# Optimization experiments

Hardware: AMD Instinct MI355X
Metric: run time of the kernel (lower is better)

The kernel has to match this reference:

```python
import jax, jax.numpy as jnp
import numpy as np

N_NODES = 50000
N_EDGES = 400000
IN_DIM = 256
HID = 64
N_CLASSES = 121


def setup_inputs() -> dict:
    key = jax.random.key(0)
    ks = jax.random.split(key, 16)
    inp = {
        "features": jax.random.normal(ks[0], (N_NODES, IN_DIM), jnp.float32),
        "src": jax.random.randint(ks[1], (N_EDGES,), 0, N_NODES, jnp.int32),
        "dst": jax.random.randint(ks[2], (N_EDGES,), 0, N_NODES, jnp.int32),
        # layer 0: 4 heads, in_dim -> hid, no residual
        "W0": jax.random.normal(ks[3], (4, HID, IN_DIM), jnp.float32) * 0.05,
        "al0": jax.random.normal(ks[4], (4, HID), jnp.float32) * 0.05,
        "ar0": jax.random.normal(ks[5], (4, HID), jnp.float32) * 0.05,
        # layer 1: 4 heads, 4*hid -> hid, residual via fc
        "W1": jax.random.normal(ks[6], (4, HID, 4 * HID), jnp.float32) * 0.05,
        "al1": jax.random.normal(ks[7], (4, HID), jnp.float32) * 0.05,
        "ar1": jax.random.normal(ks[8], (4, HID), jnp.float32) * 0.05,
        "R1": jax.random.normal(ks[9], (4, HID, 4 * HID), jnp.float32) * 0.05,
        # final: 6 heads, 4*hid -> classes, residual via fc, averaged
        "Wf": jax.random.normal(ks[10], (6, N_CLASSES, 4 * HID), jnp.float32) * 0.05,
        "alf": jax.random.normal(ks[11], (6, N_CLASSES), jnp.float32) * 0.05,
        "arf": jax.random.normal(ks[12], (6, N_CLASSES), jnp.float32) * 0.05,
        "Rf": jax.random.normal(ks[13], (6, N_CLASSES, 4 * HID), jnp.float32) * 0.05,
    }
    return inp


def _gat_layer(x, src, dst, W, al, ar, R, n_nodes):
    """Multi-head GAT layer. x:[N,D], W:[H,K,D], al/ar:[H,K], R:[H,K,D] or None.
    Returns [N,H,K] = activation(residual + edge-softmax-weighted neighbor sum)."""
    ft = jnp.einsum('nd,hkd->nhk', x, W)              # [N,H,K]
    a1 = jnp.einsum('nhk,hk->nh', ft, al)             # [N,H] attn_l(ft)
    a2 = jnp.einsum('nhk,hk->nh', ft, ar)             # [N,H] attn_r(ft)
    # per-edge score: leaky_relu(a1[dst] + a2[src]) (DGL mailbox softmax over in-edges)
    s = jax.nn.leaky_relu(a1[dst] + a2[src], negative_slope=0.01)   # [E,H]
    smax = jax.ops.segment_max(s, dst, num_segments=n_nodes)        # [N,H]
    smax = jnp.where(jnp.isfinite(smax), smax, 0.0)
    ex = jnp.exp(s - smax[dst])                                     # [E,H]
    denom = jax.ops.segment_sum(ex, dst, num_segments=n_nodes)      # [N,H]
    msg = ex[:, :, None] * ft[src]                                  # [E,H,K]
    accum = jax.ops.segment_sum(msg, dst, num_segments=n_nodes)     # [N,H,K]
    accum = accum / jnp.where(denom > 0, denom, 1.0)[:, :, None]
    if R is not None:
        accum = accum + jnp.einsum('nd,hkd->nhk', x, R)
    return jax.nn.elu(accum)


def reference(features, src, dst, W0, al0, ar0, W1, al1, ar1, R1, Wf, alf, arf, Rf):
    n = features.shape[0]
    h0 = _gat_layer(features, src, dst, W0, al0, ar0, None, n)  # [N,4,64]
    h0 = h0.reshape(n, -1)                                      # concat heads -> [N,256]
    h1 = _gat_layer(h0, src, dst, W1, al1, ar1, R1, n)          # [N,4,64]
    h1 = h1.reshape(n, -1)                                      # [N,256]
    hf = _gat_layer(h1, src, dst, Wf, alf, arf, Rf, n)          # [N,6,121]
    return hf.mean(axis=1)                                      # average final heads -> [N,121]
```

## Files before the change

### kernel.cpp

```cpp
#include <hip/hip_runtime.h>
#include <math.h>

#define NN 50000
#define NE 400000
#define NB ((NN + 255) / 256)

typedef __attribute__((ext_vector_type(8))) short bf16x8;
typedef __attribute__((ext_vector_type(4))) float f32x4;
#define AS1 __attribute__((address_space(1)))
#define AS3 __attribute__((address_space(3)))

__device__ __forceinline__ float lrelu(float x){ return x > 0.0f ? x : 0.01f*x; }
__device__ __forceinline__ float eluf(float x){ return x > 0.0f ? x : __expf(x)-1.0f; }
__device__ __forceinline__ float bf2f(unsigned short u){
  union{unsigned i; float f;} v; v.i = ((unsigned)u)<<16; return v.f;
}
__device__ __forceinline__ unsigned short f2bf(float x){
  union{float f; unsigned i;} v; v.f = x;
  unsigned r = v.i + 0x7FFFu + ((v.i>>16)&1u);
  return (unsigned short)(r>>16);
}
__device__ __forceinline__ unsigned pack2(float a, float b){
  return (unsigned)f2bf(a) | ((unsigned)f2bf(b)<<16);
}
__device__ __forceinline__ float lo16(unsigned u){ return bf2f((unsigned short)(u & 0xffffu)); }
__device__ __forceinline__ float hi16(unsigned u){ return bf2f((unsigned short)(u >> 16)); }

__global__ void k_diag(float* out, float val){ out[0] = val; }

__global__ void k_cvt(const float* __restrict__ in, unsigned short* __restrict__ o, int n){
  int i = (blockIdx.x*256 + threadIdx.x)*4;
  if(i + 3 < n){
    float4 v = *(const float4*)(in + i);
    uint2 p; p.x = pack2(v.x, v.y); p.y = pack2(v.z, v.w);
    *(uint2*)(o + i) = p;
  } else {
    for(int k = i; k < n; k++) o[k] = f2bf(in[k]);
  }
}

__global__ void k_cvt3(const float* __restrict__ s0, const float* __restrict__ s1,
    const float* __restrict__ s2, unsigned short* __restrict__ d0,
    unsigned short* __restrict__ d1, unsigned short* __restrict__ d2, int n){
  const float* in = (blockIdx.y == 0) ? s0 : (blockIdx.y == 1) ? s1 : s2;
  unsigned short* o = (blockIdx.y == 0) ? d0 : (blockIdx.y == 1) ? d1 : d2;
  int i = (blockIdx.x*256 + threadIdx.x)*4;
  if(i + 3 < n){
    float4 v = *(const float4*)(in + i);
    uint2 p; p.x = pack2(v.x, v.y); p.y = pack2(v.z, v.w);
    *(uint2*)(o + i) = p;
  } else {
    for(int k = i; k < n; k++) o[k] = f2bf(in[k]);
  }
}

__global__ void k_cvt2(const float* __restrict__ s0, const float* __restrict__ s1,
    unsigned short* __restrict__ d0, unsigned short* __restrict__ d1, int n){
  const float* in = (blockIdx.y == 0) ? s0 : s1;
  unsigned short* o = (blockIdx.y == 0) ? d0 : d1;
  int i = (blockIdx.x*256 + threadIdx.x)*4;
  if(i + 3 < n){
    float4 v = *(const float4*)(in + i);
    uint2 p; p.x = pack2(v.x, v.y); p.y = pack2(v.z, v.w);
    *(uint2*)(o + i) = p;
  } else {
    for(int k = i; k < n; k++) o[k] = f2bf(in[k]);
  }
}

__global__ void k_fold(const float* __restrict__ W, const float* __restrict__ al,
    const float* __restrict__ ar, float* __restrict__ fl, float* __restrict__ fr, int K){
  int h = blockIdx.x, d = threadIdx.x;
  float sl = 0.f, sr = 0.f;
  const float* wb = W + ((size_t)h*K)*256 + d;
  for(int k = 0; k < K; k++){
    float w = wb[(size_t)k*256];
    sl += al[h*K + k]*w;
    sr += ar[h*K + k]*w;
  }
  fl[h*256 + d] = sl;
  fr[h*256 + d] = sr;
}

__global__ void k_count(const int* __restrict__ dst, int* __restrict__ cnt, int E){
  int e = blockIdx.x * 256 + threadIdx.x;
  if(e < E) atomicAdd(&cnt[dst[e]], 1);
}

__global__ void k_scanA(const int* __restrict__ cnt, int* __restrict__ row_ptr,
    int* __restrict__ bsum, int N){
  __shared__ int sh[256];
  int t = threadIdx.x;
  int i = blockIdx.x*256 + t;
  int v = (i < N) ? cnt[i] : 0;
  sh[t] = v;
  __syncthreads();
  for(int off = 1; off < 256; off <<= 1){
    int u = (t >= off) ? sh[t - off] : 0;
    __syncthreads();
    sh[t] += u;
    __syncthreads();
  }
  if(i < N) row_ptr[i] = sh[t] - v;
  if(t == 255) bsum[blockIdx.x] = sh[255];
}

__global__ void k_scanB(const int* __restrict__ bsum, int* __restrict__ boff, int nb){
  __shared__ int sh[256];
  int t = threadIdx.x;
  int v = (t < nb) ? bsum[t] : 0;
  sh[t] = v;
  __syncthreads();
  for(int off = 1; off < 256; off <<= 1){
    int u = (t >= off) ? sh[t - off] : 0;
    __syncthreads();
    sh[t] += u;
    __syncthreads();
  }
  if(t < nb) boff[t] = sh[t] - v;
  if(t == 255) boff[nb] = sh[255];
}

__global__ void k_scanC(int* __restrict__ row_ptr, const int* __restrict__ boff, int N, int nb){
  int i = blockIdx.x*256 + threadIdx.x;
  if(i < N) row_ptr[i] += boff[blockIdx.x];
  if(i == 0) row_ptr[N] = boff[nb];
}

__global__ void k_scatter(const int* __restrict__ src, const int* __restrict__ dst,
    const int* __restrict__ row_ptr, int* __restrict__ cur, int* __restrict__ col_src, int E){
  int e = blockIdx.x * 256 + threadIdx.x;
  if(e < E){
    int d = dst[e];
    int pos = row_ptr[d] + atomicAdd(&cur[d], 1);
    col_src[pos] = src[e];
  }
}

__global__ __launch_bounds__(256) void k_gemm16(const unsigned short* __restrict__ X,
    const unsigned short* __restrict__ W, unsigned short* __restrict__ out,
    int N, int Kout, int ostride){
  __shared__ unsigned short sA[4096];
  __shared__ unsigned short sB[4096];
  int tid = threadIdx.x;
  int l = tid & 63, w = tid >> 6;
  int wm = w >> 1, wn = w & 1;
  int row0 = blockIdx.x*128, col0 = blockIdx.y*128;

  f32x4 acc[4][4];
  #pragma unroll
  for(int i=0;i<4;i++)
    #pragma unroll
    for(int j=0;j<4;j++) acc[i][j] = (f32x4){0.f,0.f,0.f,0.f};

  int grA0 = row0 + l;        if(grA0 >= N) grA0 = 0;
  int grA1 = row0 + 64 + l;   if(grA1 >= N) grA1 = 0;
  int gcB0 = col0 + l;        if(gcB0 >= Kout) gcB0 = 0;
  int gcB1 = col0 + 64 + l;   if(gcB1 >= Kout) gcB1 = 0;
  const unsigned short* pa0 = X + (size_t)grA0*256 + w*8;
  const unsigned short* pa1 = X + (size_t)grA1*256 + w*8;
  const unsigned short* pb0 = W + (size_t)gcB0*256 + w*8;
  const unsigned short* pb1 = W + (size_t)gcB1*256 + w*8;

  AS3 unsigned short* a3A = (AS3 unsigned short*)sA;
  AS3 unsigned short* a3B = (AS3 unsigned short*)sB;

  for(int kt = 0; kt < 256; kt += 32){
    __builtin_amdgcn_global_load_lds((const AS1 void*)(pa0 + kt), (AS3 void*)(a3A + w*1024),       16, 0, 0);
    __builtin_amdgcn_global_load_lds((const AS1 void*)(pa1 + kt), (AS3 void*)(a3A + w*1024 + 512), 16, 0, 0);
    __builtin_amdgcn_global_load_lds((const AS1 void*)(pb0 + kt), (AS3 void*)(a3B + w*1024),       16, 0, 0);
    __builtin_amdgcn_global_load_lds((const AS1 void*)(pb1 + kt), (AS3 void*)(a3B + w*1024 + 512), 16, 0, 0);
    __syncthreads();
    bf16x8 af[4], bfr[4];
    #pragma unroll
    for(int f=0; f<4; f++){
      af[f]  = *(const bf16x8*)(sA + (l>>4)*1024 + (wm*64 + f*16 + (l&15))*8);
      bfr[f] = *(const bf16x8*)(sB + (l>>4)*1024 + (wn*64 + f*16 + (l&15))*8);
    }
    #pragma unroll
    for(int i=0;i<4;i++)
      #pragma unroll
      for(int j=0;j<4;j++)
        acc[i][j] = __builtin_amdgcn_mfma_f32_16x16x32_bf16(af[i], bfr[j], acc[i][j], 0, 0, 0);
    __syncthreads();
  }

  #pragma unroll
  for(int i=0;i<4;i++){
    int rbase = row0 + wm*64 + i*16 + (l>>4)*4;
    #pragma unroll
    for(int j=0;j<4;j++){
      int c = col0 + wn*64 + j*16 + (l&15);
      if(c < Kout){
        #pragma unroll
        for(int q=0;q<4;q++){
          int r = rbase + q;
          if(r < N) out[(size_t)r*ostride + c] = f2bf(acc[i][j][q]);
        }
      }
    }
  }
}

__global__ __launch_bounds__(256) void k_gemmFh(const unsigned short* __restrict__ aggX,
    const unsigned short* __restrict__ xin, const unsigned short* __restrict__ wf,
    const unsigned short* __restrict__ rf, float* __restrict__ partial, int M){
  __shared__ unsigned short sA[4096];
  __shared__ unsigned short sB[4096];
  int tid = threadIdx.x;
  int l = tid & 63, w = tid >> 6;
  int wm = w >> 1, wn = w & 1;
  int h = blockIdx.y;
  int row0 = blockIdx.x*128;
  int rA0 = row0 + l;      if(rA0 >= M) rA0 = 0;
  int rA1 = row0 + 64 + l; if(rA1 >= M) rA1 = 0;
  int cB1 = 64 + l; if(cB1 > 120) cB1 = 120;

  AS3 unsigned short* a3A = (AS3 unsigned short*)sA;
  AS3 unsigned short* a3B = (AS3 unsigned short*)sB;

  f32x4 acc[4][4];
  #pragma unroll
  for(int i=0;i<4;i++)
    #pragma unroll
    for(int j=0;j<4;j++) acc[i][j] = (f32x4){0.f,0.f,0.f,0.f};

  #pragma unroll 1
  for(int ph = 0; ph < 2; ph++){
    const unsigned short* pa0 = (ph ? xin + (size_t)rA0*256 : aggX + (size_t)rA0*1536 + h*256) + w*8;
    const unsigned short* pa1 = (ph ? xin + (size_t)rA1*256 : aggX + (size_t)rA1*1536 + h*256) + w*8;
    const unsigned short* pbb = (ph ? rf : wf) + (size_t)h*121*256;
    const unsigned short* pb0 = pbb + (size_t)l*256 + w*8;
    const unsigned short* pb1 = pbb + (size_t)cB1*256 + w*8;
    for(int kt = 0; kt < 256; kt += 32){
      __builtin_amdgcn_global_load_lds((const AS1 void*)(pa0 + kt), (AS3 void*)(a3A + w*1024),       16, 0, 0);
      __builtin_amdgcn_global_load_lds((const AS1 void*)(pa1 + kt), (AS3 void*)(a3A + w*1024 + 512), 16, 0, 0);
      __builtin_amdgcn_global_load_lds((const AS1 void*)(pb0 + kt), (AS3 void*)(a3B + w*1024),       16, 0, 0);
      __builtin_amdgcn_global_load_lds((const AS1 void*)(pb1 + kt), (AS3 void*)(a3B + w*1024 + 512), 16, 0, 0);
      __syncthreads();
      bf16x8 af[4], bfr[4];
      #pragma unroll
      for(int f=0; f<4; f++){
        af[f]  = *(const bf16x8*)(sA + (l>>4)*1024 + (wm*64 + f*16 + (l&15))*8);
        bfr[f] = *(const bf16x8*)(sB + (l>>4)*1024 + (wn*64 + f*16 + (l&15))*8);
      }
      #pragma unroll
      for(int i=0;i<4;i++)
        #pragma unroll
        for(int j=0;j<4;j++)
          acc[i][j] = __builtin_amdgcn_mfma_f32_16x16x32_bf16(af[i], bfr[j], acc[i][j], 0, 0, 0);
      __syncthreads();
    }
  }

  float* pb = partial + (size_t)h*M*128;
  #pragma unroll
  for(int i=0;i<4;i++){
    int rbase = row0 + wm*64 + i*16 + (l>>4)*4;
    #pragma unroll
    for(int j=0;j<4;j++){
      int c = wn*64 + j*16 + (l&15);
      #pragma unroll
      for(int q=0;q<4;q++){
        int r = rbase + q;
        if(r < M) pb[(size_t)r*128 + c] = eluf(acc[i][j][q]);
      }
    }
  }
}

__global__ __launch_bounds__(256) void k_reduce6(const float* __restrict__ partial,
    float* __restrict__ outp, int n0, int M){
  int t = blockIdx.x*256 + threadIdx.x;
  int idx = t >> 7, c = t & 127;
  if(idx >= M || c >= 121) return;
  float s = 0.f;
  #pragma unroll
  for(int h = 0; h < 6; h++) s += partial[((size_t)h*M + idx)*128 + c];
  outp[(size_t)(n0 + idx)*121 + c] = s * (1.0f/6.0f);
}

template<int H, int OS>
__global__ __launch_bounds__(256) void k_a12dot(const unsigned short* __restrict__ x,
    const float* __restrict__ fl, const float* __restrict__ fr,
    float* __restrict__ a1, float* __restrict__ a2){
  int n = blockIdx.x*4 + (threadIdx.x>>6);
  if(n >= NN) return;
  int l = threadIdx.x & 63;
  uint2 rv = *(const uint2*)(x + (size_t)n*256 + l*4);
  float c0 = lo16(rv.x), c1 = hi16(rv.x), c2 = lo16(rv.y), c3 = hi16(rv.y);
  float s1[H], s2[H];
  #pragma unroll
  for(int h = 0; h < H; h++){
    float4 vl = *(const float4*)(fl + h*256 + l*4);
    float4 vr = *(const float4*)(fr + h*256 + l*4);
    s1[h] = c0*vl.x + c1*vl.y + c2*vl.z + c3*vl.w;
    s2[h] = c0*vr.x + c1*vr.y + c2*vr.z + c3*vr.w;
  }
  #pragma unroll
  for(int off = 32; off > 0; off >>= 1){
    #pragma unroll
    for(int h = 0; h < H; h++){
      s1[h] += __shfl_xor(s1[h], off);
      s2[h] += __shfl_xor(s2[h], off);
    }
  }
  if(l == 0){
    #pragma unroll
    for(int h = 0; h < H; h++){ a1[(size_t)n*OS + h] = s1[h]; a2[(size_t)n*OS + h] = s2[h]; }
  }
}

template<bool HAS_RES>
__global__ __launch_bounds__(256) void k_agg4(const unsigned short* __restrict__ ft, int fts,
    const float* __restrict__ a1, const float* __restrict__ a2,
    const int* __restrict__ row_ptr, const int* __restrict__ col_src,
    const unsigned short* __restrict__ res, int rs, unsigned short* __restrict__ outp){
  int n = blockIdx.x*4 + (threadIdx.x>>6);
  if(n >= NN) return;
  int l = threadIdx.x & 63;
  int h = l >> 4;
  int e0 = row_ptr[n], e1 = row_ptr[n+1];
  float a1v = a1[n*4 + h];
  float acc0=0.f, acc1=0.f, acc2=0.f, acc3=0.f, d=0.f;
  int e = e0;
  for(; e + 4 <= e1; e += 4){
    int s0 = col_src[e], s1 = col_src[e+1], s2 = col_src[e+2], s3 = col_src[e+3];
    float sc0 = a2[(size_t)s0*4 + h];
    float sc1 = a2[(size_t)s1*4 + h];
    float sc2 = a2[(size_t)s2*4 + h];
    float sc3 = a2[(size_t)s3*4 + h];
    uint2 r0 = *(const uint2*)(ft + (size_t)s0*fts + l*4);
    uint2 r1 = *(const uint2*)(ft + (size_t)s1*fts + l*4);
    uint2 r2 = *(const uint2*)(ft + (size_t)s2*fts + l*4);
    uint2 r3 = *(const uint2*)(ft + (size_t)s3*fts + l*4);
    float x0 = __expf(lrelu(a1v + sc0));
    float x1 = __expf(lrelu(a1v + sc1));
    float x2 = __expf(lrelu(a1v + sc2));
    float x3 = __expf(lrelu(a1v + sc3));
    d += (x0 + x1) + (x2 + x3);
    acc0 += x0*lo16(r0.x) + x1*lo16(r1.x) + x2*lo16(r2.x) + x3*lo16(r3.x);
    acc1 += x0*hi16(r0.x) + x1*hi16(r1.x) + x2*hi16(r2.x) + x3*hi16(r3.x);
    acc2 += x0*lo16(r0.y) + x1*lo16(r1.y) + x2*lo16(r2.y) + x3*lo16(r3.y);
    acc3 += x0*hi16(r0.y) + x1*hi16(r1.y) + x2*hi16(r2.y) + x3*hi16(r3.y);
  }
  for(; e < e1; ++e){
    int s = col_src[e];
    float x = __expf(lrelu(a1v + a2[(size_t)s*4 + h]));
    d += x;
    uint2 rv = *(const uint2*)(ft + (size_t)s*fts + l*4);
    acc0 += x*lo16(rv.x); acc1 += x*hi16(rv.x);
    acc2 += x*lo16(rv.y); acc3 += x*hi16(rv.y);
  }
  float inv = (e1 > e0) ? 1.0f/d : 0.0f;
  float v0 = acc0*inv, v1 = acc1*inv, v2 = acc2*inv, v3 = acc3*inv;
  if(HAS_RES){
    uint2 rr = *(const uint2*)(res + (size_t)n*rs + l*4);
    v0 += lo16(rr.x); v1 += hi16(rr.x); v2 += lo16(rr.y); v3 += hi16(rr.y);
  }
  uint2 o;
  o.x = pack2(eluf(v0), eluf(v1));
  o.y = pack2(eluf(v2), eluf(v3));
  *(uint2*)(outp + (size_t)n*256 + l*4) = o;
}

__global__ __launch_bounds__(256) void k_aggx6(const unsigned short* __restrict__ x,
    const float* __restrict__ a1, const float* __restrict__ a2,
    const int* __restrict__ row_ptr, const int* __restrict__ col_src,
    unsigned short* __restrict__ aggX, int n0base, int M){
  int idx = blockIdx.x*4 + (threadIdx.x>>6);
  if(idx >= M) return;
  int n = n0base + idx;
  int l = threadIdx.x & 63;
  int e0 = row_ptr[n], e1 = row_ptr[n+1];
  float a1v[6];
  #pragma unroll
  for(int h=0;h<6;h++) a1v[h] = a1[(size_t)n*8 + h];
  float acc[6][4];
  float d[6];
  #pragma unroll
  for(int h=0;h<6;h++){ d[h]=0.f; acc[h][0]=0.f; acc[h][1]=0.f; acc[h][2]=0.f; acc[h][3]=0.f; }
  int e = e0;
  for(; e + 2 <= e1; e += 2){
    int s0 = col_src[e], s1 = col_src[e+1];
    float4 alo0 = *(const float4*)(a2 + (size_t)s0*8);
    float2 ahi0 = *(const float2*)(a2 + (size_t)s0*8 + 4);
    float4 alo1 = *(const float4*)(a2 + (size_t)s1*8);
    float2 ahi1 = *(const float2*)(a2 + (size_t)s1*8 + 4);
    uint2 rv0 = *(const uint2*)(x + (size_t)s0*256 + l*4);
    uint2 rv1 = *(const uint2*)(x + (size_t)s1*256 + l*4);
    float ex0[6], ex1[6];
    ex0[0] = __expf(lrelu(a1v[0] + alo0.x));
    ex0[1] = __expf(lrelu(a1v[1] + alo0.y));
    ex0[2] = __expf(lrelu(a1v[2] + alo0.z));
    ex0[3] = __expf(lrelu(a1v[3] + alo0.w));
    ex0[4] = __expf(lrelu(a1v[4] + ahi0.x));
    ex0[5] = __expf(lrelu(a1v[5] + ahi0.y));
    ex1[0] = __expf(lrelu(a1v[0] + alo1.x));
    ex1[1] = __expf(lrelu(a1v[1] + alo1.y));
    ex1[2] = __expf(lrelu(a1v[2] + alo1.z));
    ex1[3] = __expf(lrelu(a1v[3] + alo1.w));
    ex1[4] = __expf(lrelu(a1v[4] + ahi1.x));
    ex1[5] = __expf(lrelu(a1v[5] + ahi1.y));
    float c00 = lo16(rv0.x), c01 = hi16(rv0.x), c02 = lo16(rv0.y), c03 = hi16(rv0.y);
    float c10 = lo16(rv1.x), c11 = hi16(rv1.x), c12 = lo16(rv1.y), c13 = hi16(rv1.y);
    #pragma unroll
    for(int h=0;h<6;h++){
      d[h] += ex0[h] + ex1[h];
      acc[h][0] += ex0[h]*c00 + ex1[h]*c10;
      acc[h][1] += ex0[h]*c01 + ex1[h]*c11;
      acc[h][2] += ex0[h]*c02 + ex1[h]*c12;
      acc[h][3] += ex0[h]*c03 + ex1[h]*c13;
    }
  }
  for(; e < e1; ++e){
    int s = col_src[e];
    float4 alo = *(const float4*)(a2 + (size_t)s*8);
    float2 ahi = *(const float2*)(a2 + (size_t)s*8 + 4);
    uint2 rv = *(const uint2*)(x + (size_t)s*256 + l*4);
    float ex[6];
    ex[0] = __expf(lrelu(a1v[0] + alo.x));
    ex[1] = __expf(lrelu(a1v[1] + alo.y));
    ex[2] = __expf(lrelu(a1v[2] + alo.z));
    ex[3] = __expf(lrelu(a1v[3] + alo.w));
    ex[4] = __expf(lrelu(a1v[4] + ahi.x));
    ex[5] = __expf(lrelu(a1v[5] + ahi.y));
    float c0 = lo16(rv.x), c1 = hi16(rv.x), c2 = lo16(rv.y), c3 = hi16(rv.y);
    #pragma unroll
    for(int h=0;h<6;h++){
      d[h] += ex[h];
      acc[h][0] += ex[h]*c0;
      acc[h][1] += ex[h]*c1;
      acc[h][2] += ex[h]*c2;
      acc[h][3] += ex[h]*c3;
    }
  }
  bool deg = e1 > e0;
  #pragma unroll
  for(int h=0;h<6;h++){
    float inv = deg ? 1.0f/d[h] : 0.0f;
    uint2 o;
    o.x = pack2(acc[h][0]*inv, acc[h][1]*inv);
    o.y = pack2(acc[h][2]*inv, acc[h][3]*inv);
    *(uint2*)(aggX + (size_t)idx*1536 + h*256 + l*4) = o;
  }
}

extern "C" void kernel_launch(void* const* d_in, const int* in_sizes, int n_in,
                              void* d_out, int out_size, void* d_ws, size_t ws_size,
                              hipStream_t stream){
  const float* features = (const float*)d_in[0];
  const int*   src      = (const int*)d_in[1];
  const int*   dst      = (const int*)d_in[2];
  const float* W0  = (const float*)d_in[3];
  const float* al0 = (const float*)d_in[4];
  const float* ar0 = (const float*)d_in[5];
  const float* W1  = (const float*)d_in[6];
  const float* al1 = (const float*)d_in[7];
  const float* ar1 = (const float*)d_in[8];
  const float* R1  = (const float*)d_in[9];
  const float* Wf  = (const float*)d_in[10];
  const float* alf = (const float*)d_in[11];
  const float* arf = (const float*)d_in[12];
  const float* Rf  = (const float*)d_in[13];
  float* out = (float*)d_out;
  (void)in_sizes; (void)n_in; (void)out_size;

  char* ws = (char*)d_ws;
  size_t off = 0;
  auto take = [&](size_t bytes) -> void* {
    void* p = ws + off;
    off += (bytes + 255) & ~(size_t)255;
    return p;
  };
  const int CH = 25000;
  int* row_ptr = (int*)take((NN + 1) * sizeof(int));
  int* cur     = (int*)take(NN * sizeof(int));
  int* col_src = (int*)take(NE * sizeof(int));
  int* bsum    = (int*)take(256 * sizeof(int));
  int* boff    = (int*)take(257 * sizeof(int));
  float* a1 = (float*)take((size_t)NN * 8 * sizeof(float));
  float* a2 = (float*)take((size_t)NN * 8 * sizeof(float));
  unsigned short* ftres  = (unsigned short*)take((size_t)NN * 512 * 2);
  unsigned short* feat16 = (unsigned short*)take((size_t)NN * 256 * 2);
  unsigned short* hA16   = (unsigned short*)take((size_t)NN * 256 * 2);
  unsigned short* hB16   = (unsigned short*)take((size_t)NN * 256 * 2);
  unsigned short* aggX   = (unsigned short*)take((size_t)CH * 1536 * 2);
  unsigned short* w016  = (unsigned short*)take(65536 * 2);
  unsigned short* w1r1  = (unsigned short*)take(131072 * 2);
  unsigned short* wf16  = (unsigned short*)take(185856 * 2);
  unsigned short* rf16  = (unsigned short*)take(185856 * 2);
  float* fl0 = (float*)take(4*256*sizeof(float));
  float* fr0 = (float*)take(4*256*sizeof(float));
  float* fl1 = (float*)take(4*256*sizeof(float));
  float* fr1 = (float*)take(4*256*sizeof(float));
  float* flF = (float*)take(6*256*sizeof(float));
  float* frF = (float*)take(6*256*sizeof(float));
  size_t need = off;

  if(ws_size < need){
    k_diag<<<1, 1, 0, stream>>>(out, 100.0f + (float)((double)ws_size / 1073741824.0));
    return;
  }

  float* partialF = (float*)ftres;

  hipMemsetAsync(cur, 0, NN * sizeof(int), stream);
  k_count<<<(NE + 255)/256, 256, 0, stream>>>(dst, cur, NE);
  k_scanA<<<NB, 256, 0, stream>>>(cur, row_ptr, bsum, NN);
  k_scanB<<<1, 256, 0, stream>>>(bsum, boff, NB);
  k_scanC<<<NB, 256, 0, stream>>>(row_ptr, boff, NN, NB);
  hipMemsetAsync(cur, 0, NN * sizeof(int), stream);
  k_scatter<<<(NE + 255)/256, 256, 0, stream>>>(src, dst, row_ptr, cur, col_src, NE);

  k_cvt<<<(NN*256/4 + 255)/256, 256, 0, stream>>>(features, feat16, NN*256);
  k_cvt3<<<dim3(64, 3), 256, 0, stream>>>(W0, W1, R1, w016, w1r1, w1r1 + 65536, 65536);
  k_cvt2<<<dim3(182, 2), 256, 0, stream>>>(Wf, Rf, wf16, rf16, 185856);
  k_fold<<<4, 256, 0, stream>>>(W0, al0, ar0, fl0, fr0, 64);
  k_fold<<<4, 256, 0, stream>>>(W1, al1, ar1, fl1, fr1, 64);
  k_fold<<<6, 256, 0, stream>>>(Wf, alf, arf, flF, frF, 121);

  int gm = (NN + 127) / 128;
  int gagg = (NN + 3) / 4;

  k_a12dot<4,4><<<gagg, 256, 0, stream>>>(feat16, fl0, fr0, a1, a2);
  k_gemm16<<<dim3(gm, 2), 256, 0, stream>>>(feat16, w016, ftres, NN, 256, 256);
  k_agg4<false><<<gagg, 256, 0, stream>>>(ftres, 256, a1, a2, row_ptr, col_src, nullptr, 0, hA16);

  k_a12dot<4,4><<<gagg, 256, 0, stream>>>(hA16, fl1, fr1, a1, a2);
  k_gemm16<<<dim3(gm, 4), 256, 0, stream>>>(hA16, w1r1, ftres, NN, 512, 512);
  k_agg4<true><<<gagg, 256, 0, stream>>>(ftres, 512, a1, a2, row_ptr, col_src, ftres + 256, 512, hB16);

  k_a12dot<6,8><<<gagg, 256, 0, stream>>>(hB16, flF, frF, a1, a2);
  for(int c = 0; c < 2; c++){
    int n0 = c*CH;
    k_aggx6<<<(CH + 3)/4, 256, 0, stream>>>(hB16, a1, a2, row_ptr, col_src, aggX, n0, CH);
    k_gemmFh<<<dim3((CH + 127)/128, 6), 256, 0, stream>>>(aggX, hB16 + (size_t)n0*256, wf16, rf16, partialF, CH);
    k_reduce6<<<(CH*128 + 255)/256, 256, 0, stream>>>(partialF, out, n0, CH);
  }
}
```

Baseline: 605.2 us.

## Fuse next-layer attention dots into aggregation; bf16 partials; merge fold kernels

The next layer's attention logits (a1/a2) are now computed inside the aggregation kernel from the fp32 ELU outputs, removing two separate a12dot passes that re-read the 256-wide bf16 features. Double-buffered a1/a2 arrays avoid a read/write hazard between layers. The final-head partial results are stored as bf16 instead of fp32, halving that write and the reduce-kernel read at some cost in precision. The three fold launches are merged into one.

Measured after the change: 517.7 us. 1.17x faster.

```diff
diff --git a/kernel.cpp b/kernel.cpp
--- a/kernel.cpp
+++ b/kernel.cpp
@@ -68,9 +68,16 @@
   }
 }
 
-__global__ void k_fold(const float* __restrict__ W, const float* __restrict__ al,
-    const float* __restrict__ ar, float* __restrict__ fl, float* __restrict__ fr, int K){
-  int h = blockIdx.x, d = threadIdx.x;
+__global__ void k_foldAll(const float* __restrict__ W0, const float* __restrict__ al0, const float* __restrict__ ar0,
+    const float* __restrict__ W1, const float* __restrict__ al1, const float* __restrict__ ar1,
+    const float* __restrict__ Wf, const float* __restrict__ alf, const float* __restrict__ arf,
+    float* __restrict__ fl0, float* __restrict__ fr0, float* __restrict__ fl1, float* __restrict__ fr1,
+    float* __restrict__ flF, float* __restrict__ frF){
+  int b = blockIdx.x, d = threadIdx.x;
+  const float *W, *al, *ar; float *fl, *fr; int K, h;
+  if(b < 4){ W=W0; al=al0; ar=ar0; fl=fl0; fr=fr0; K=64; h=b; }
+  else if(b < 8){ W=W1; al=al1; ar=ar1; fl=fl1; fr=fr1; K=64; h=b-4; }
+  else { W=Wf; al=alf; ar=arf; fl=flF; fr=frF; K=121; h=b-8; }
   float sl = 0.f, sr = 0.f;
   const float* wb = W + ((size_t)h*K)*256 + d;
   for(int k = 0; k < K; k++){
@@ -204,7 +211,7 @@
 
 __global__ __launch_bounds__(256) void k_gemmFh(const unsigned short* __restrict__ aggX,
     const unsigned short* __restrict__ xin, const unsigned short* __restrict__ wf,
-    const unsigned short* __restrict__ rf, float* __restrict__ partial, int M){
+    const unsigned short* __restrict__ rf, unsigned short* __restrict__ partial, int M){
   __shared__ unsigned short sA[4096];
   __shared__ unsigned short sB[4096];
   int tid = threadIdx.x;
@@ -253,7 +260,7 @@
     }
   }
 
-  float* pb = partial + (size_t)h*M*128;
+  unsigned short* pb = partial + (size_t)h*M*128;
   #pragma unroll
   for(int i=0;i<4;i++){
     int rbase = row0 + wm*64 + i*16 + (l>>4)*4;
@@ -263,20 +270,20 @@
       #pragma unroll
       for(int q=0;q<4;q++){
         int r = rbase + q;
-        if(r < M) pb[(size_t)r*128 + c] = eluf(acc[i][j][q]);
+        if(r < M) pb[(size_t)r*128 + c] = f2bf(eluf(acc[i][j][q]));
       }
     }
   }
 }
 
-__global__ __launch_bounds__(256) void k_reduce6(const float* __restrict__ partial,
+__global__ __launch_bounds__(256) void k_reduce6(const unsigned short* __restrict__ partial,
     float* __restrict__ outp, int n0, int M){
   int t = blockIdx.x*256 + threadIdx.x;
   int idx = t >> 7, c = t & 127;
   if(idx >= M || c >= 121) return;
   float s = 0.f;
   #pragma unroll
-  for(int h = 0; h < 6; h++) s += partial[((size_t)h*M + idx)*128 + c];
+  for(int h = 0; h < 6; h++) s += bf2f(partial[((size_t)h*M + idx)*128 + c]);
   outp[(size_t)(n0 + idx)*121 + c] = s * (1.0f/6.0f);
 }
 
@@ -311,11 +318,13 @@
   }
 }
 
-template<bool HAS_RES>
+template<bool HAS_RES, int NH, int NOS>
 __global__ __launch_bounds__(256) void k_agg4(const unsigned short* __restrict__ ft, int fts,
     const float* __restrict__ a1, const float* __restrict__ a2,
     const int* __restrict__ row_ptr, const int* __restrict__ col_src,
-    const unsigned short* __restrict__ res, int rs, unsigned short* __restrict__ outp){
+    const unsigned short* __restrict__ res, int rs, unsigned short* __restrict__ outp,
+    const float* __restrict__ nfl, const float* __restrict__ nfr,
+    float* __restrict__ na1, float* __restrict__ na2){
   int n = blockIdx.x*4 + (threadIdx.x>>6);
   if(n >= NN) return;
   int l = threadIdx.x & 63;
@@ -358,10 +367,35 @@
     uint2 rr = *(const uint2*)(res + (size_t)n*rs + l*4);
     v0 += lo16(rr.x); v1 += hi16(rr.x); v2 += lo16(rr.y); v3 += hi16(rr.y);
   }
+  float o0 = eluf(v0), o1 = eluf(v1), o2 = eluf(v2), o3 = eluf(v3);
   uint2 o;
-  o.x = pack2(eluf(v0), eluf(v1));
-  o.y = pack2(eluf(v2), eluf(v3));
+  o.x = pack2(o0, o1);
+  o.y = pack2(o2, o3);
   *(uint2*)(outp + (size_t)n*256 + l*4) = o;
+
+  float s1[NH], s2[NH];
+  #pragma unroll
+  for(int hh = 0; hh < NH; hh++){
+    float4 vl = *(const float4*)(nfl + hh*256 + l*4);
+    float4 vr = *(const float4*)(nfr + hh*256 + l*4);
+    s1[hh] = o0*vl.x + o1*vl.y + o2*vl.z + o3*vl.w;
+    s2[hh] = o0*vr.x + o1*vr.y + o2*vr.z + o3*vr.w;
+  }
+  #pragma unroll
+  for(int off = 32; off > 0; off >>= 1){
+    #pragma unroll
+    for(int hh = 0; hh < NH; hh++){
+      s1[hh] += __shfl_xor(s1[hh], off);
+      s2[hh] += __shfl_xor(s2[hh], off);
+    }
+  }
+  if(l == 0){
+    #pragma unroll
+    for(int hh = 0; hh < NH; hh++){
+      na1[(size_t)n*NOS + hh] = s1[hh];
+      na2[(size_t)n*NOS + hh] = s2[hh];
+    }
+  }
 }
 
 __global__ __launch_bounds__(256) void k_aggx6(const unsigned short* __restrict__ x,
@@ -479,8 +513,10 @@
   int* col_src = (int*)take(NE * sizeof(int));
   int* bsum    = (int*)take(256 * sizeof(int));
   int* boff    = (int*)take(257 * sizeof(int));
-  float* a1 = (float*)take((size_t)NN * 8 * sizeof(float));
-  float* a2 = (float*)take((size_t)NN * 8 * sizeof(float));
+  float* a1A = (float*)take((size_t)NN * 8 * sizeof(float));
+  float* a2A = (float*)take((size_t)NN * 8 * sizeof(float));
+  float* a1B = (float*)take((size_t)NN * 8 * sizeof(float));
+  float* a2B = (float*)take((size_t)NN * 8 * sizeof(float));
   unsigned short* ftres  = (unsigned short*)take((size_t)NN * 512 * 2);
   unsigned short* feat16 = (unsigned short*)take((size_t)NN * 256 * 2);
   unsigned short* hA16   = (unsigned short*)take((size_t)NN * 256 * 2);
@@ -503,7 +539,7 @@
     return;
   }
 
-  float* partialF = (float*)ftres;
+  unsigned short* partialF = ftres;
 
   hipMemsetAsync(cur, 0, NN * sizeof(int), stream);
   k_count<<<(NE + 255)/256, 256, 0, stream>>>(dst, cur, NE);
@@ -516,25 +552,24 @@
   k_cvt<<<(NN*256/4 + 255)/256, 256, 0, stream>>>(features, feat16, NN*256);
   k_cvt3<<<dim3(64, 3), 256, 0, stream>>>(W0, W1, R1, w016, w1r1, w1r1 + 65536, 65536);
   k_cvt2<<<dim3(182, 2), 256, 0, stream>>>(Wf, Rf, wf16, rf16, 185856);
-  k_fold<<<4, 256, 0, stream>>>(W0, al0, ar0, fl0, fr0, 64);
-  k_fold<<<4, 256, 0, stream>>>(W1, al1, ar1, fl1, fr1, 64);
-  k_fold<<<6, 256, 0, stream>>>(Wf, alf, arf, flF, frF, 121);
+  k_foldAll<<<14, 256, 0, stream>>>(W0, al0, ar0, W1, al1, ar1, Wf, alf, arf,
+                                    fl0, fr0, fl1, fr1, flF, frF);
 
   int gm = (NN + 127) / 128;
   int gagg = (NN + 3) / 4;
 
-  k_a12dot<4,4><<<gagg, 256, 0, stream>>>(feat16, fl0, fr0, a1, a2);
+  k_a12dot<4,4><<<gagg, 256, 0, stream>>>(feat16, fl0, fr0, a1A, a2A);
   k_gemm16<<<dim3(gm, 2), 256, 0, stream>>>(feat16, w016, ftres, NN, 256, 256);
-  k_agg4<false><<<gagg, 256, 0, stream>>>(ftres, 256, a1, a2, row_ptr, col_src, nullptr, 0, hA16);
-
-  k_a12dot<4,4><<<gagg, 256, 0, stream>>>(hA16, fl1, fr1, a1, a2);
+  k_agg4<false,4,4><<<gagg, 256, 0, stream>>>(ftres, 256, a1A, a2A, row_ptr, col_src,
+      nullptr, 0, hA16, fl1, fr1, a1B, a2B);
+
   k_gemm16<<<dim3(gm, 4), 256, 0, stream>>>(hA16, w1r1, ftres, NN, 512, 512);
-  k_agg4<true><<<gagg, 256, 0, stream>>>(ftres, 512, a1, a2, row_ptr, col_src, ftres + 256, 512, hB16);
-
-  k_a12dot<6,8><<<gagg, 256, 0, stream>>>(hB16, flF, frF, a1, a2);
+  k_agg4<true,6,8><<<gagg, 256, 0, stream>>>(ftres, 512, a1B, a2B, row_ptr, col_src,
+      ftres + 256, 512, hB16, flF, frF, a1A, a2A);
+
   for(int c = 0; c < 2; c++){
     int n0 = c*CH;
-    k_aggx6<<<(CH + 3)/4, 256, 0, stream>>>(hB16, a1, a2, row_ptr, col_src, aggX, n0, CH);
+    k_aggx6<<<(CH + 3)/4, 256, 0, stream>>>(hB16, a1A, a2A, row_ptr, col_src, aggX, n0, CH);
     k_gemmFh<<<dim3((CH + 127)/128, 6), 256, 0, stream>>>(aggX, hB16 + (size_t)n0*256, wf16, rf16, partialF, CH);
     k_reduce6<<<(CH*128 + 255)/256, 256, 0, stream>>>(partialF, out, n0, CH);
   }
```
